# Optimization experiments

Measured on AMD Instinct MI355X. Metric: run time of the kernel, lower is better.

## Reference

```python
import jax, jax.numpy as jnp
import numpy as np

N_NODES = 50000
N_EDGES = 800000
N_CLASS = 16
EMB = 32
HID = 32
MSG = 32
ITERS = 6
N_GRAPHS = 50


def _linear_init(key, out_f, in_f):
    k1, k2 = jax.random.split(key)
    bound = 1.0 / np.sqrt(in_f)
    W = jax.random.uniform(k1, (out_f, in_f), jnp.float32, -bound, bound)
    b = jax.random.uniform(k2, (out_f,), jnp.float32, -bound, bound)
    return W, b


def setup_inputs() -> dict:
    key = jax.random.key(0)
    ks = jax.random.split(key, 16)
    pos = jax.random.normal(ks[0], (N_NODES, 3), jnp.float32)
    classes = jax.random.normal(ks[1], (N_NODES, N_CLASS), jnp.float32)
    edges = jax.random.randint(ks[2], (2, N_EDGES), 0, N_NODES, jnp.int32)
    W_in, b_in = _linear_init(ks[3], EMB, N_CLASS)
    W1, b1 = _linear_init(ks[4], HID, 2 * EMB + 3)
    W2, b2 = _linear_init(ks[5], HID, HID)
    W3, b3 = _linear_init(ks[6], MSG, HID)
    # torch GRUCell params: weight_ih [3H, in], weight_hh [3H, H], biases [3H], gate order r,z,n
    Wih_n, bih_n = _linear_init(ks[7], 3 * EMB, MSG)
    Whh_n, bhh_n = _linear_init(ks[8], 3 * EMB, EMB)
    Wih_e, bih_e = _linear_init(ks[9], 3 * EMB, MSG)
    Whh_e, bhh_e = _linear_init(ks[10], 3 * EMB, EMB)
    return dict(pos=pos, classes=classes, edges=edges, n_graphs=N_GRAPHS,
                W_in=W_in, b_in=b_in, W1=W1, b1=b1, W2=W2, b2=b2, W3=W3, b3=b3,
                Wih_n=Wih_n, Whh_n=Whh_n, bih_n=bih_n, bhh_n=bhh_n,
                Wih_e=Wih_e, Whh_e=Whh_e, bih_e=bih_e, bhh_e=bhh_e)


def _gru_cell(x, h, Wih, Whh, bih, bhh):
    gi = x @ Wih.T + bih
    gh = h @ Whh.T + bhh
    i_r, i_z, i_n = jnp.split(gi, 3, axis=1)
    h_r, h_z, h_n = jnp.split(gh, 3, axis=1)
    r = jax.nn.sigmoid(i_r + h_r)
    z = jax.nn.sigmoid(i_z + h_z)
    n = jnp.tanh(i_n + r * h_n)
    return (1.0 - z) * n + z * h


def reference(pos, classes, edges, n_graphs, W_in, b_in, W1, b1, W2, b2, W3, b3,
              Wih_n, Whh_n, bih_n, bhh_n, Wih_e, Whh_e, bih_e, bhh_e):
    n_nodes = classes.shape[0]
    n_edge = edges.shape[1]
    node = classes @ W_in.T + b_in                      # [N, 32]
    esym = jnp.concatenate([edges, edges[::-1]], axis=1)  # [2, 2E]
    d_pos = pos[esym[1]] - pos[esym[0]]                 # [2E, 3]
    edge_feat = (node[edges[0]] + node[edges[1]]) * 0.5  # [E, 32]
    for _ in range(ITERS):
        src = node[esym[0]]                             # [2E, 32]
        dst = node[esym[1]]                             # [2E, 32]
        x = jnp.concatenate([src, dst, d_pos], axis=1)  # [2E, 67]
        m = jax.nn.relu(x @ W1.T + b1)
        m = jax.nn.relu(m @ W2.T + b2)
        m = m @ W3.T + b3                               # [2E, 32]
        a = jax.ops.segment_sum(m, esym[0], num_segments=n_nodes)  # [N, 32]
        node = _gru_cell(a, node, Wih_n, Whh_n, bih_n, bhh_n)
        b = (m[:n_edge] + m[n_edge:]) * 0.5             # [E, 32]
        edge_feat = _gru_cell(b, edge_feat, Wih_e, Whh_e, bih_e, bhh_e)
    # equal-size graphs: split + pad reduces to a reshape
    return node.reshape(n_graphs, n_nodes // n_graphs, node.shape[1])
```

## Files before the change

kernel.cpp:

```cpp
#include <hip/hip_runtime.h>


#define NN      50000
#define NE      800000
#define NE2     (2 * NE)
#define NCLS    16
#define NBLK    196

typedef short s8v __attribute__((ext_vector_type(8)));
typedef float f4v __attribute__((ext_vector_type(4)));
typedef unsigned short u16;

__device__ __forceinline__ unsigned rne16(float f) {
    unsigned u = __float_as_uint(f);
    return (u + 0x7FFFu + ((u >> 16) & 1u)) >> 16;
}
__device__ __forceinline__ unsigned pkbf(float lo, float hi) {
    return rne16(lo) | (rne16(hi) << 16);
}
__device__ __forceinline__ s8v pack8(const float* f) {
    s8v r;
#pragma unroll
    for (int i = 0; i < 8; ++i) r[i] = (short)rne16(f[i]);
    return r;
}
__device__ __forceinline__ float gru1(float gr, float gz, float gin, float ghn,
                                      float h) {
    float r  = __builtin_amdgcn_rcpf(1.0f + __expf(-gr));
    float z  = __builtin_amdgcn_rcpf(1.0f + __expf(-gz));
    float pre = fmaf(r, ghn, gin);
    float nj = 1.0f - 2.0f * __builtin_amdgcn_rcpf(1.0f + __expf(2.0f * pre));
    return fmaf(z, h - nj, nj);
}

__global__ __launch_bounds__(256) void prep_kernel(
    const float* __restrict__ Wih, const float* __restrict__ Whh,
    const float* __restrict__ bih, const float* __restrict__ bhh,
    const float* __restrict__ W1, const float* __restrict__ b1,
    u16* __restrict__ Wg_bf, float* __restrict__ bg, float* __restrict__ W1p,
    u16* __restrict__ Wp_bf)
{
    int idx = blockIdx.x * 256 + threadIdx.x;
    if (idx < 8192) {
        int o = idx >> 6, k = idx & 63;
        float val;
        if (o < 64) {
            val = (k < 32) ? Wih[o * 32 + k] : Whh[o * 32 + (k - 32)];
        } else if (o < 96) {
            val = (k < 32) ? Wih[o * 32 + k] : 0.0f;
        } else {
            val = (k >= 32) ? Whh[(o - 32) * 32 + (k - 32)] : 0.0f;
        }
        Wg_bf[idx] = (u16)rne16(val);
    } else if (idx < 8320) {
        int i = idx - 8192;
        float val;
        if (i < 64)       val = bih[i] + bhh[i];
        else if (i < 96)  val = bih[i];
        else              val = bhh[i - 32];
        bg[i] = val;
    } else if (idx < 8448) {
        int t = idx - 8320;
        int j = t >> 2, c = t & 3;
        W1p[t] = (c < 3) ? W1[j * 67 + 64 + c] : b1[j];
    } else if (idx < 10496) {
        int t = idx - 8448;
        int r = t >> 5, k = t & 31;
        float val = (r < 32) ? W1[r * 67 + k] : W1[(r - 32) * 67 + 32 + k];
        Wp_bf[t] = (u16)rne16(val);
    }
}

__global__ __launch_bounds__(256) void hist_rank_kernel(
    const int* __restrict__ e0, const int* __restrict__ e1,
    int* __restrict__ deg, int* __restrict__ rank)
{
    int e = blockIdx.x * 256 + threadIdx.x;
    int s = (e < NE) ? e0[e] : e1[e - NE];
    rank[e] = atomicAdd(&deg[s], 1);
}

__global__ __launch_bounds__(256) void scan_part_kernel(
    const int* __restrict__ deg, int* __restrict__ bsum)
{
    int t = blockIdx.x * 256 + threadIdx.x;
    int x = (t < NN) ? deg[t] : 0;
#pragma unroll
    for (int off = 1; off < 64; off <<= 1) x += __shfl_xor(x, off);
    __shared__ int wsum[4];
    if ((threadIdx.x & 63) == 0) wsum[threadIdx.x >> 6] = x;
    __syncthreads();
    if (threadIdx.x == 0)
        bsum[blockIdx.x] = wsum[0] + wsum[1] + wsum[2] + wsum[3];
}

__global__ __launch_bounds__(256) void scan_mid_kernel(
    const int* __restrict__ bsum, int* __restrict__ boff, int* __restrict__ rowptr)
{
    __shared__ int sd[256];
    int t = threadIdx.x;
    int x = (t < NBLK) ? bsum[t] : 0;
    sd[t] = x;
    __syncthreads();
    for (int off = 1; off < 256; off <<= 1) {
        int vv = (t >= off) ? sd[t - off] : 0;
        __syncthreads();
        sd[t] += vv;
        __syncthreads();
    }
    if (t < NBLK) boff[t] = sd[t] - x;
    if (t == 0) rowptr[NN] = NE2;
}

__global__ __launch_bounds__(256) void scan_apply_kernel(
    const int* __restrict__ deg, const int* __restrict__ boff,
    int* __restrict__ rowptr)
{
    __shared__ int sd[256];
    int tid = threadIdx.x;
    int t = blockIdx.x * 256 + tid;
    int x = (t < NN) ? deg[t] : 0;
    sd[tid] = x;
    __syncthreads();
    for (int off = 1; off < 256; off <<= 1) {
        int vv = (tid >= off) ? sd[tid - off] : 0;
        __syncthreads();
        sd[tid] += vv;
        __syncthreads();
    }
    if (t < NN) rowptr[t] = boff[blockIdx.x] + sd[tid] - x;
}

__global__ __launch_bounds__(256) void scatter_kernel(
    const int* __restrict__ e0, const int* __restrict__ e1,
    const int* __restrict__ rowptr, const int* __restrict__ rank,
    int2* __restrict__ sd)
{
    int e = blockIdx.x * 256 + threadIdx.x;
    int s, d;
    if (e < NE) { s = e0[e]; d = e1[e]; }
    else        { s = e1[e - NE]; d = e0[e - NE]; }
    int p = rowptr[s] + rank[e];
    sd[p] = make_int2(s, d);
}

__device__ __forceinline__ void proj_uv(const float nn[32], int n,
                                        const float* __restrict__ W1,
                                        float* __restrict__ u, float* __restrict__ v)
{
    for (int j = 0; j < 32; ++j) {
        float su = 0.0f, sv = 0.0f;
#pragma unroll
        for (int k = 0; k < 32; ++k) {
            su = fmaf(W1[j * 67 + k],      nn[k], su);
            sv = fmaf(W1[j * 67 + 32 + k], nn[k], sv);
        }
        u[(size_t)n * 32 + j] = su;
        v[(size_t)n * 32 + j] = sv;
    }
}

__global__ __launch_bounds__(256) void init_kernel(
    const float* __restrict__ classes, const float* __restrict__ W_in,
    const float* __restrict__ b_in, const float* __restrict__ W1,
    float* __restrict__ node, float* __restrict__ u, float* __restrict__ v,
    float* __restrict__ acc)
{
    int n = blockIdx.x * 256 + threadIdx.x;
    if (n >= NN) return;

    float cls[16];
    const float4* cr = reinterpret_cast<const float4*>(classes + (size_t)n * NCLS);
#pragma unroll
    for (int q = 0; q < 4; ++q) {
        float4 c4 = cr[q];
        cls[q * 4 + 0] = c4.x; cls[q * 4 + 1] = c4.y;
        cls[q * 4 + 2] = c4.z; cls[q * 4 + 3] = c4.w;
    }

    float nn[32];
#pragma unroll
    for (int j = 0; j < 32; ++j) {
        float t = b_in[j];
#pragma unroll
        for (int k = 0; k < 16; ++k) t = fmaf(W_in[j * 16 + k], cls[k], t);
        nn[j] = t;
        node[(size_t)n * 32 + j] = t;
    }

    float4 z4 = make_float4(0.f, 0.f, 0.f, 0.f);
    float4* aw = reinterpret_cast<float4*>(acc + (size_t)n * 32);
#pragma unroll
    for (int q = 0; q < 8; ++q) aw[q] = z4;

    proj_uv(nn, n, W1, u, v);
}

#define H1STEP(j, uu, vv)                                                            \
    {                                                                                \
        float pre = fmaf(dx, W1p[(j) * 4 + 0], (uu) + (vv));                         \
        pre = fmaf(dy, W1p[(j) * 4 + 1], pre);                                       \
        pre = fmaf(dz, W1p[(j) * 4 + 2], pre);                                       \
        pre += W1p[(j) * 4 + 3];                                                     \
        h1[j] = fmaxf(pre, 0.0f);                                                    \
    }

__global__ __launch_bounds__(256, 4) void edge_kernel(
    const int2* __restrict__ sd, const float* __restrict__ pos,
    const float* __restrict__ u, const float* __restrict__ v,
    const float* __restrict__ W1p,
    const float* __restrict__ W2, const float* __restrict__ b2,
    const float* __restrict__ W3, const float* __restrict__ b3,
    float* __restrict__ acc)
{
    __shared__ int slds[256];
    __shared__ __align__(16) char uni[18432];
    unsigned (*stag)[1024] = (unsigned (*)[1024])uni;
    float (*mld)[36] = (float (*)[36])uni;

    int tid = threadIdx.x;
    int wv = tid >> 6, lane = tid & 63;
    int l15 = lane & 15, l4 = lane >> 4;

    s8v w2f[2], w3f[2];
    f4v b2v[2], b3v[2];
#pragma unroll
    for (int mt = 0; mt < 2; ++mt) {
        const float* p2 = W2 + (mt * 16 + l15) * 32 + l4 * 8;
        const float* p3 = W3 + (mt * 16 + l15) * 32 + l4 * 8;
        float4 a0 = *(const float4*)p2;
        float4 a1 = *(const float4*)(p2 + 4);
        float4 c0 = *(const float4*)p3;
        float4 c1 = *(const float4*)(p3 + 4);
        s8v w2x, w3x;
        w2x[0] = (short)rne16(a0.x); w2x[1] = (short)rne16(a0.y);
        w2x[2] = (short)rne16(a0.z); w2x[3] = (short)rne16(a0.w);
        w2x[4] = (short)rne16(a1.x); w2x[5] = (short)rne16(a1.y);
        w2x[6] = (short)rne16(a1.z); w2x[7] = (short)rne16(a1.w);
        w3x[0] = (short)rne16(c0.x); w3x[1] = (short)rne16(c0.y);
        w3x[2] = (short)rne16(c0.z); w3x[3] = (short)rne16(c0.w);
        w3x[4] = (short)rne16(c1.x); w3x[5] = (short)rne16(c1.y);
        w3x[6] = (short)rne16(c1.z); w3x[7] = (short)rne16(c1.w);
        w2f[mt] = w2x; w3f[mt] = w3x;
        b2v[mt] = *(const f4v*)(b2 + mt * 16 + l4 * 4);
        b3v[mt] = *(const f4v*)(b3 + mt * 16 + l4 * 4);
    }

    int e = blockIdx.x * 256 + tid;
    int2 p = sd[e];
    int s = p.x, d = p.y;
    slds[tid] = s;

    float dx = pos[d * 3 + 0] - pos[s * 3 + 0];
    float dy = pos[d * 3 + 1] - pos[s * 3 + 1];
    float dz = pos[d * 3 + 2] - pos[s * 3 + 2];

    const float4* ur = reinterpret_cast<const float4*>(u + (size_t)s * 32);
    const float4* vr = reinterpret_cast<const float4*>(v + (size_t)d * 32);

    float h1[32];
#pragma unroll
    for (int q = 0; q < 8; ++q) {
        float4 uq = ur[q];
        float4 vq = vr[q];
        H1STEP(q * 4 + 0, uq.x, vq.x);
        H1STEP(q * 4 + 1, uq.y, vq.y);
        H1STEP(q * 4 + 2, uq.z, vq.z);
        H1STEP(q * 4 + 3, uq.w, vq.w);
    }

#pragma unroll
    for (int c = 0; c < 4; ++c) {
        uint4 q;
        q.x = pkbf(h1[c * 8 + 0], h1[c * 8 + 1]);
        q.y = pkbf(h1[c * 8 + 2], h1[c * 8 + 3]);
        q.z = pkbf(h1[c * 8 + 4], h1[c * 8 + 5]);
        q.w = pkbf(h1[c * 8 + 6], h1[c * 8 + 7]);
        *(uint4*)&stag[wv][c * 256 + lane * 4] = q;
    }
    asm volatile("s_waitcnt lgkmcnt(0)" ::: "memory");

    s8v bf[4];
#pragma unroll
    for (int t = 0; t < 4; ++t)
        bf[t] = *(const s8v*)&stag[wv][l4 * 256 + (t * 16 + l15) * 4];

    f4v h2a[2][4];
#pragma unroll
    for (int mt = 0; mt < 2; ++mt)
#pragma unroll
        for (int t = 0; t < 4; ++t)
            h2a[mt][t] = __builtin_amdgcn_mfma_f32_16x16x32_bf16(
                w2f[mt], bf[t], b2v[mt], 0, 0, 0);

#pragma unroll
    for (int mt = 0; mt < 2; ++mt) {
        int kc = mt * 2 + (l4 >> 1);
#pragma unroll
        for (int t = 0; t < 4; ++t) {
            float e0 = fmaxf(h2a[mt][t][0], 0.0f);
            float e1 = fmaxf(h2a[mt][t][1], 0.0f);
            float e2 = fmaxf(h2a[mt][t][2], 0.0f);
            float e3 = fmaxf(h2a[mt][t][3], 0.0f);
            uint2 w; w.x = pkbf(e0, e1); w.y = pkbf(e2, e3);
            *(uint2*)&stag[wv][kc * 256 + (t * 16 + l15) * 4 + (l4 & 1) * 2] = w;
        }
    }
    asm volatile("s_waitcnt lgkmcnt(0)" ::: "memory");

#pragma unroll
    for (int t = 0; t < 4; ++t)
        bf[t] = *(const s8v*)&stag[wv][l4 * 256 + (t * 16 + l15) * 4];
    asm volatile("s_waitcnt lgkmcnt(0)" ::: "memory");
    __syncthreads();

    f4v ma[2][4];
#pragma unroll
    for (int mt = 0; mt < 2; ++mt)
#pragma unroll
        for (int t = 0; t < 4; ++t)
            ma[mt][t] = __builtin_amdgcn_mfma_f32_16x16x32_bf16(
                w3f[mt], bf[t], b3v[mt], 0, 0, 0);

    int c = tid & 31, g = tid >> 5;

    if (wv < 2) {
#pragma unroll
        for (int mt = 0; mt < 2; ++mt)
#pragma unroll
            for (int t = 0; t < 4; ++t)
                *(f4v*)&mld[wv * 64 + t * 16 + l15][mt * 16 + l4 * 4] = ma[mt][t];
    }
    __syncthreads();
    {
        int base = g * 16;
        int scur = slds[base];
        float sum = 0.0f;
        for (int r = 0; r < 16; ++r) {
            int row = base + r;
            int sr = slds[row];
            if (sr != scur) {
                unsafeAtomicAdd(&acc[(size_t)scur * 32 + c], sum);
                sum = 0.0f;
                scur = sr;
            }
            sum += mld[row][c];
        }
        unsafeAtomicAdd(&acc[(size_t)scur * 32 + c], sum);
    }
    __syncthreads();

    if (wv >= 2) {
#pragma unroll
        for (int mt = 0; mt < 2; ++mt)
#pragma unroll
            for (int t = 0; t < 4; ++t)
                *(f4v*)&mld[(wv - 2) * 64 + t * 16 + l15][mt * 16 + l4 * 4] = ma[mt][t];
    }
    __syncthreads();
    {
        int base = 128 + g * 16;
        int scur = slds[base];
        float sum = 0.0f;
        for (int r = 0; r < 16; ++r) {
            int row = base + r;
            int sr = slds[row];
            if (sr != scur) {
                unsafeAtomicAdd(&acc[(size_t)scur * 32 + c], sum);
                sum = 0.0f;
                scur = sr;
            }
            sum += mld[row - 128][c];
        }
        unsafeAtomicAdd(&acc[(size_t)scur * 32 + c], sum);
    }
}

__global__ __launch_bounds__(64) void node_mfma_kernel(
    float* __restrict__ node, float* __restrict__ acc,
    const u16* __restrict__ Wg_bf, const float* __restrict__ bg,
    const u16* __restrict__ Wp_bf,
    float* __restrict__ u, float* __restrict__ v, int last)
{
    __shared__ short stag[8][64][8];
    __shared__ float hlds[64][36];

    int lane = threadIdx.x;
    int l15 = lane & 15, l4 = lane >> 4;
    int base = blockIdx.x * 64;
    int xg = base + lane;
    bool xv = xg < NN;

    float a[32], h[32];
    if (xv) {
        const f4v* ar = (const f4v*)(acc + (size_t)xg * 32);
        const f4v* hr = (const f4v*)(node + (size_t)xg * 32);
#pragma unroll
        for (int q = 0; q < 8; ++q) {
            f4v t4 = ar[q];
            a[q*4+0] = t4[0]; a[q*4+1] = t4[1]; a[q*4+2] = t4[2]; a[q*4+3] = t4[3];
            f4v s4 = hr[q];
            h[q*4+0] = s4[0]; h[q*4+1] = s4[1]; h[q*4+2] = s4[2]; h[q*4+3] = s4[3];
        }
        f4v z4 = {0.f, 0.f, 0.f, 0.f};
        f4v* aw = (f4v*)(acc + (size_t)xg * 32);
#pragma unroll
        for (int q = 0; q < 8; ++q) aw[q] = z4;
    } else {
#pragma unroll
        for (int q = 0; q < 32; ++q) { a[q] = 0.0f; h[q] = 0.0f; }
    }
#pragma unroll
    for (int kc = 0; kc < 4; ++kc) {
        *(s8v*)&stag[kc][lane][0]     = pack8(&a[kc * 8]);
        *(s8v*)&stag[4 + kc][lane][0] = pack8(&h[kc * 8]);
    }
#pragma unroll
    for (int q = 0; q < 8; ++q) {
        f4v hv = {h[q*4+0], h[q*4+1], h[q*4+2], h[q*4+3]};
        *(f4v*)&hlds[lane][q * 4] = hv;
    }
    asm volatile("s_waitcnt lgkmcnt(0)" ::: "memory");
    __builtin_amdgcn_sched_barrier(0);

    s8v wa0[8], wa1[8];
    f4v bias[8];
#pragma unroll
    for (int mt = 0; mt < 8; ++mt) {
        int row = mt * 16 + l15;
        wa0[mt]  = *(const s8v*)(Wg_bf + row * 64 + l4 * 8);
        wa1[mt]  = *(const s8v*)(Wg_bf + row * 64 + 32 + l4 * 8);
        bias[mt] = *(const f4v*)(bg + mt * 16 + l4 * 4);
    }

#pragma unroll
    for (int nt = 0; nt < 4; ++nt) {
        s8v b0 = *(const s8v*)&stag[l4][nt * 16 + l15][0];
        s8v b1 = *(const s8v*)&stag[4 + l4][nt * 16 + l15][0];
        f4v g[8];
#pragma unroll
        for (int mt = 0; mt < 8; ++mt) {
            f4v cacc = __builtin_amdgcn_mfma_f32_16x16x32_bf16(wa0[mt], b0,
                                                               bias[mt], 0, 0, 0);
            g[mt] = __builtin_amdgcn_mfma_f32_16x16x32_bf16(wa1[mt], b1,
                                                            cacc, 0, 0, 0);
        }
        int nd = nt * 16 + l15;
        f4v hv0 = *(f4v*)&hlds[nd][4 * l4];
        f4v hv1 = *(f4v*)&hlds[nd][16 + 4 * l4];
        f4v o0, o1;
#pragma unroll
        for (int r = 0; r < 4; ++r) {
            o0[r] = gru1(g[0][r], g[2][r], g[4][r], g[6][r], hv0[r]);
            o1[r] = gru1(g[1][r], g[3][r], g[5][r], g[7][r], hv1[r]);
        }
        *(f4v*)&hlds[nd][4 * l4] = o0;
        *(f4v*)&hlds[nd][16 + 4 * l4] = o1;
    }
    asm volatile("s_waitcnt lgkmcnt(0)" ::: "memory");
    __builtin_amdgcn_sched_barrier(0);

    float nn[32];
#pragma unroll
    for (int q = 0; q < 8; ++q) {
        f4v t4 = *(f4v*)&hlds[lane][q * 4];
        nn[q*4+0] = t4[0]; nn[q*4+1] = t4[1]; nn[q*4+2] = t4[2]; nn[q*4+3] = t4[3];
    }
    if (xv) {
        f4v* nw = (f4v*)(node + (size_t)xg * 32);
#pragma unroll
        for (int q = 0; q < 8; ++q) {
            f4v t4 = {nn[q*4+0], nn[q*4+1], nn[q*4+2], nn[q*4+3]};
            nw[q] = t4;
        }
    }
    if (last) return;

#pragma unroll
    for (int kc = 0; kc < 4; ++kc)
        *(s8v*)&stag[kc][lane][0] = pack8(&nn[kc * 8]);
    asm volatile("s_waitcnt lgkmcnt(0)" ::: "memory");
    __builtin_amdgcn_sched_barrier(0);

#pragma unroll
    for (int nt = 0; nt < 4; ++nt) {
        s8v b = *(const s8v*)&stag[l4][nt * 16 + l15][0];
        int nd = base + nt * 16 + l15;
        bool nv = nd < NN;
#pragma unroll
        for (int mt = 0; mt < 4; ++mt) {
            s8v aa = *(const s8v*)(Wp_bf + (mt * 16 + l15) * 32 + l4 * 8);
            f4v cz = {0.f, 0.f, 0.f, 0.f};
            f4v pr = __builtin_amdgcn_mfma_f32_16x16x32_bf16(aa, b, cz, 0, 0, 0);
            if (nv) {
                float* dst = (mt < 2)
                    ? (u + (size_t)nd * 32 + mt * 16 + 4 * l4)
                    : (v + (size_t)nd * 32 + (mt - 2) * 16 + 4 * l4);
                *(f4v*)dst = pr;
            }
        }
    }
}

extern "C" void kernel_launch(void* const* d_in, const int* in_sizes, int n_in,
                              void* d_out, int out_size, void* d_ws, size_t ws_size,
                              hipStream_t stream)
{
    const float* pos     = (const float*)d_in[0];
    const float* classes = (const float*)d_in[1];
    const int*   edges   = (const int*)d_in[2];
    const float* W_in = (const float*)d_in[4];
    const float* b_in = (const float*)d_in[5];
    const float* W1   = (const float*)d_in[6];
    const float* b1   = (const float*)d_in[7];
    const float* W2   = (const float*)d_in[8];
    const float* b2   = (const float*)d_in[9];
    const float* W3   = (const float*)d_in[10];
    const float* b3   = (const float*)d_in[11];
    const float* Wih_n = (const float*)d_in[12];
    const float* Whh_n = (const float*)d_in[13];
    const float* bih_n = (const float*)d_in[14];
    const float* bhh_n = (const float*)d_in[15];

    float* node = (float*)d_out;

    float* ws  = (float*)d_ws;
    float* u   = ws;
    float* v   = u + (size_t)NN * 32;
    float* acc = v + (size_t)NN * 32;
    float* bg  = acc + (size_t)NN * 32;
    float* W1p = bg + 128;
    u16* Wg_bf = (u16*)(W1p + 128);
    u16* Wp_bf = Wg_bf + 8192;
    int* bsum   = (int*)(Wp_bf + 2048);
    int* boff   = bsum + 256;
    int* deg    = boff + 256;
    int* rank   = deg + NN;
    int* rowptr = rank + NE2;
    uintptr_t sp = (uintptr_t)(rowptr + NN + 1);
    sp = (sp + 255) & ~(uintptr_t)255;
    int2* sd = (int2*)sp;

    const int* e0 = edges;
    const int* e1 = edges + NE;

    prep_kernel<<<41, 256, 0, stream>>>(Wih_n, Whh_n, bih_n, bhh_n, W1, b1,
                                        Wg_bf, bg, W1p, Wp_bf);
    hipMemsetAsync(deg, 0, (size_t)NN * sizeof(int), stream);
    hist_rank_kernel<<<NE2 / 256, 256, 0, stream>>>(e0, e1, deg, rank);
    scan_part_kernel<<<NBLK, 256, 0, stream>>>(deg, bsum);
    scan_mid_kernel<<<1, 256, 0, stream>>>(bsum, boff, rowptr);
    scan_apply_kernel<<<NBLK, 256, 0, stream>>>(deg, boff, rowptr);
    scatter_kernel<<<NE2 / 256, 256, 0, stream>>>(e0, e1, rowptr, rank, sd);
    init_kernel<<<NBLK, 256, 0, stream>>>(classes, W_in, b_in, W1,
                                          node, u, v, acc);
    for (int it = 0; it < 6; ++it) {
        edge_kernel<<<NE2 / 256, 256, 0, stream>>>(sd, pos, u, v, W1p,
                                                   W2, b2, W3, b3, acc);
        node_mfma_kernel<<<(NN + 63) / 64, 64, 0, stream>>>(node, acc, Wg_bf, bg,
                                                            Wp_bf, u, v, it == 5);
    }
}
```

Before: 777.1 us.

## Replace LDS-staged segmented reduction with in-register shuffle segmented scan

```diff
diff --git a/kernel.cpp b/kernel.cpp
--- a/kernel.cpp
+++ b/kernel.cpp
@@ -213,10 +213,7 @@
     const float* __restrict__ W3, const float* __restrict__ b3,
     float* __restrict__ acc)
 {
-    __shared__ int slds[256];
-    __shared__ __align__(16) char uni[18432];
-    unsigned (*stag)[1024] = (unsigned (*)[1024])uni;
-    float (*mld)[36] = (float (*)[36])uni;
+    __shared__ unsigned stag[4][1024];
 
     int tid = threadIdx.x;
     int wv = tid >> 6, lane = tid & 63;
@@ -249,7 +246,6 @@
     int e = blockIdx.x * 256 + tid;
     int2 p = sd[e];
     int s = p.x, d = p.y;
-    slds[tid] = s;
 
     float dx = pos[d * 3 + 0] - pos[s * 3 + 0];
     float dy = pos[d * 3 + 1] - pos[s * 3 + 1];
@@ -279,6 +275,7 @@
         *(uint4*)&stag[wv][c * 256 + lane * 4] = q;
     }
     asm volatile("s_waitcnt lgkmcnt(0)" ::: "memory");
+    __builtin_amdgcn_sched_barrier(0);
 
     s8v bf[4];
 #pragma unroll
@@ -307,12 +304,11 @@
         }
     }
     asm volatile("s_waitcnt lgkmcnt(0)" ::: "memory");
+    __builtin_amdgcn_sched_barrier(0);
 
 #pragma unroll
     for (int t = 0; t < 4; ++t)
         bf[t] = *(const s8v*)&stag[wv][l4 * 256 + (t * 16 + l15) * 4];
-    asm volatile("s_waitcnt lgkmcnt(0)" ::: "memory");
-    __syncthreads();
 
     f4v ma[2][4];
 #pragma unroll
@@ -322,57 +318,35 @@
             ma[mt][t] = __builtin_amdgcn_mfma_f32_16x16x32_bf16(
                 w3f[mt], bf[t], b3v[mt], 0, 0, 0);
 
-    int c = tid & 31, g = tid >> 5;
-
-    if (wv < 2) {
-#pragma unroll
-        for (int mt = 0; mt < 2; ++mt)
-#pragma unroll
-            for (int t = 0; t < 4; ++t)
-                *(f4v*)&mld[wv * 64 + t * 16 + l15][mt * 16 + l4 * 4] = ma[mt][t];
-    }
-    __syncthreads();
-    {
-        int base = g * 16;
-        int scur = slds[base];
-        float sum = 0.0f;
-        for (int r = 0; r < 16; ++r) {
-            int row = base + r;
-            int sr = slds[row];
-            if (sr != scur) {
-                unsafeAtomicAdd(&acc[(size_t)scur * 32 + c], sum);
-                sum = 0.0f;
-                scur = sr;
+#pragma unroll
+    for (int nt = 0; nt < 4; ++nt) {
+        int st = __shfl(s, nt * 16 + l15);
+        f4v m0 = ma[0][nt], m1 = ma[1][nt];
+#pragma unroll
+        for (int k = 1; k < 16; k <<= 1) {
+            int sk = __shfl_up(st, k, 16);
+            f4v t0, t1;
+#pragma unroll
+            for (int r = 0; r < 4; ++r) {
+                t0[r] = __shfl_up(m0[r], k, 16);
+                t1[r] = __shfl_up(m1[r], k, 16);
             }
-            sum += mld[row][c];
-        }
-        unsafeAtomicAdd(&acc[(size_t)scur * 32 + c], sum);
-    }
-    __syncthreads();
-
-    if (wv >= 2) {
-#pragma unroll
-        for (int mt = 0; mt < 2; ++mt)
-#pragma unroll
-            for (int t = 0; t < 4; ++t)
-                *(f4v*)&mld[(wv - 2) * 64 + t * 16 + l15][mt * 16 + l4 * 4] = ma[mt][t];
-    }
-    __syncthreads();
-    {
-        int base = 128 + g * 16;
-        int scur = slds[base];
-        float sum = 0.0f;
-        for (int r = 0; r < 16; ++r) {
-            int row = base + r;
-            int sr = slds[row];
-            if (sr != scur) {
-                unsafeAtomicAdd(&acc[(size_t)scur * 32 + c], sum);
-                sum = 0.0f;
-                scur = sr;
+            bool addf = (l15 >= k) && (sk == st);
+#pragma unroll
+            for (int r = 0; r < 4; ++r) {
+                m0[r] += addf ? t0[r] : 0.0f;
+                m1[r] += addf ? t1[r] : 0.0f;
             }
-            sum += mld[row - 128][c];
-        }
-        unsafeAtomicAdd(&acc[(size_t)scur * 32 + c], sum);
+        }
+        int sn = __shfl_down(st, 1, 16);
+        if ((l15 == 15) || (sn != st)) {
+            float* row = acc + (size_t)st * 32 + 4 * l4;
+#pragma unroll
+            for (int r = 0; r < 4; ++r) {
+                unsafeAtomicAdd(row + r,      m0[r]);
+                unsafeAtomicAdd(row + 16 + r, m1[r]);
+            }
+        }
     }
 }
 
```

Measured after the change: 879.9 us. 1.13x slower.
